# Performance work log

Measured on AMD Instinct MI355X. Metric: run time of the kernel, lower is better.

Reference implementation:

```python
import jax, jax.numpy as jnp
import numpy as np

N_NODES = 50000
N_EDGES = 800000
BASIS = 64
HIDDEN_RO = 128
N_GRAPHS = 512
T = 3


def setup_inputs() -> dict:
    key = jax.random.key(0)
    ks = jax.random.split(key, 12)
    Z = jax.random.randint(ks[0], (N_NODES,), 0, 10)
    edge_index = jax.random.randint(ks[1], (2, N_EDGES), 0, N_NODES)
    edge_attr = jax.random.normal(ks[2], (N_EDGES, BASIS), dtype=jnp.float32)
    batch = jnp.sort(jax.random.randint(ks[3], (N_NODES,), 0, N_GRAPHS))
    s = 1.0 / np.sqrt(BASIS)
    embed = jax.random.normal(ks[4], (10, BASIS), dtype=jnp.float32)
    cfW = jax.random.uniform(ks[5], (BASIS, BASIS), jnp.float32, -s, s)
    cfb = jax.random.uniform(ks[6], (BASIS,), jnp.float32, -s, s)
    dfW = jax.random.uniform(ks[7], (BASIS, BASIS), jnp.float32, -s, s)
    dfb = jax.random.uniform(ks[8], (BASIS,), jnp.float32, -s, s)
    fcW = jax.random.uniform(ks[9], (BASIS, BASIS), jnp.float32, -s, s)  # no bias
    W1 = jax.random.uniform(ks[10], (BASIS, HIDDEN_RO), jnp.float32, -s, s)
    b1 = jnp.zeros((HIDDEN_RO,), jnp.float32)
    W2 = jax.random.uniform(ks[11], (HIDDEN_RO, 4), jnp.float32, -1.0 / np.sqrt(HIDDEN_RO), 1.0 / np.sqrt(HIDDEN_RO))
    b2 = jnp.zeros((4,), jnp.float32)
    return {"Z": Z, "edge_index": edge_index, "edge_attr": edge_attr, "batch": batch,
            "embed": embed, "cfW": cfW, "cfb": cfb, "dfW": dfW, "dfb": dfb, "fcW": fcW,
            "W1": W1, "b1": b1, "W2": W2, "b2": b2}


def reference(Z, edge_index, edge_attr, batch, embed, cfW, cfb, dfW, dfb, fcW, W1, b1, W2, b2):
    src, dst = edge_index[0], edge_index[1]  # x_j gathered from src, aggregated at dst
    C = embed[Z]  # [N, basis]
    # df(edge_attr) does not depend on C; compute once (same math, shared weights)
    d_feat = edge_attr @ dfW + dfb  # [E, basis]
    for _ in range(T):
        c_feat = C[src] @ cfW + cfb            # gather + linear  [E, basis]
        msg = jnp.tanh((c_feat * d_feat) @ fcW)  # [E, basis]
        agg = jax.ops.segment_sum(msg, dst, num_segments=N_NODES)
        C = C + agg
    h = jnp.tanh(C @ W1 + b1) @ W2 + b2        # readout MLP [N, 4]
    return jax.ops.segment_sum(h, batch, num_segments=N_GRAPHS)  # global_add_pool [G, 4]
```

## Files before the change

kernel.cpp:

```cpp
#include <hip/hip_runtime.h>
#include <math.h>

#define N_NODES   50000
#define N_EDGES   800000
#define BASIS     64
#define HIDDEN_RO 128
#define N_GRAPHS  512
#define T_ITERS   3

typedef short s8 __attribute__((ext_vector_type(8)));
typedef float f4 __attribute__((ext_vector_type(4)));

#define MFMA16(a, b, c) __builtin_amdgcn_mfma_f32_16x16x32_bf16(a, b, c, 0, 0, 0)

__device__ __forceinline__ float fast_tanh(float x) {
    float e = __expf(2.0f * x);
    return 1.0f - 2.0f / (e + 1.0f);
}

__device__ __forceinline__ f4 splat4(float x) { f4 v; v[0]=x; v[1]=x; v[2]=x; v[3]=x; return v; }

__device__ __forceinline__ void split8(const float* x, s8& hi, s8& lo) {
    union { unsigned a[4]; s8 v; } H, L;
    #pragma unroll
    for (int j = 0; j < 4; ++j) {
        float e0 = x[2*j], e1 = x[2*j+1];
        unsigned u0 = __float_as_uint(e0), u1 = __float_as_uint(e1);
        H.a[j] = (u0 >> 16) | (u1 & 0xFFFF0000u);
        float l0 = e0 - __uint_as_float(u0 & 0xFFFF0000u);
        float l1 = e1 - __uint_as_float(u1 & 0xFFFF0000u);
        L.a[j] = (__float_as_uint(l0) >> 16) | (__float_as_uint(l1) & 0xFFFF0000u);
    }
    hi = H.v; lo = L.v;
}

__device__ __forceinline__ void packW_dev(const float* __restrict__ W, s8* __restrict__ img, int t) {
    int lane = t & 63, q = lane >> 4, c = lane & 15;
    int f0 = (t >> 6) * 2;
    #pragma unroll
    for (int f = f0; f < f0 + 2; ++f) {
        int ks = f >> 2, g = f & 3;
        float tv[8];
        #pragma unroll
        for (int j = 0; j < 8; ++j)
            tv[j] = W[(ks*32 + q*8 + j) * 64 + g*16 + c];
        s8 hi, lo;
        split8(tv, hi, lo);
        img[f * 64 + lane]       = hi;
        img[(8 + f) * 64 + lane] = lo;
    }
}
__global__ void k_packW(const float* __restrict__ W0, const float* __restrict__ W1,
                        const float* __restrict__ W2, s8* __restrict__ i0,
                        s8* __restrict__ i1, s8* __restrict__ i2) {
    int b = blockIdx.x, t = threadIdx.x;
    if (b == 0) packW_dev(W0, i0, t);
    else if (b == 1) packW_dev(W1, i1, t);
    else packW_dev(W2, i2, t);
}

__global__ void k_init_hist(const int* __restrict__ Z, const float* __restrict__ embed,
                            float* __restrict__ C, const int* __restrict__ dst,
                            int* __restrict__ deg) {
    int i = blockIdx.x * blockDim.x + threadIdx.x;
    if (i < N_NODES * BASIS) { int n = i >> 6, c = i & 63; C[i] = embed[Z[n] * 64 + c]; }
    if (i < N_EDGES) atomicAdd(&deg[dst[i]], 1);
}

__global__ void k_scan(const int* __restrict__ deg, int* __restrict__ off,
                       int* __restrict__ cursor) {
    __shared__ int wsum[16];
    __shared__ int run_s;
    int t = threadIdx.x, lane = t & 63, w = t >> 6;
    if (t == 0) run_s = 0;
    __syncthreads();
    for (int base = 0; base < N_NODES; base += 1024) {
        int i = base + t;
        int v = (i < N_NODES) ? deg[i] : 0;
        int s = v;
        #pragma unroll
        for (int ofs = 1; ofs < 64; ofs <<= 1) {
            int tmp = __shfl_up(s, ofs, 64);
            if (lane >= ofs) s += tmp;
        }
        if (lane == 63) wsum[w] = s;
        __syncthreads();
        if (w == 0) {
            int x = (lane < 16) ? wsum[lane] : 0;
            #pragma unroll
            for (int ofs = 1; ofs < 16; ofs <<= 1) {
                int tmp = __shfl_up(x, ofs, 64);
                if (lane >= ofs) x += tmp;
            }
            if (lane < 16) wsum[lane] = x;
        }
        __syncthreads();
        int run = run_s;
        int wex = (w == 0) ? 0 : wsum[w - 1];
        int incl = run + wex + s;
        if (i < N_NODES) { off[i] = incl - v; cursor[i] = incl - v; }
        __syncthreads();
        if (t == 1023) run_s = incl;
        __syncthreads();
    }
    if (t == 0) off[N_NODES] = run_s;
}

__global__ void k_fill(const int* __restrict__ src, const int* __restrict__ dst,
                       int* __restrict__ cursor, int* __restrict__ slot_e,
                       int* __restrict__ slot_s) {
    int e = blockIdx.x * blockDim.x + threadIdx.x;
    if (e < N_EDGES) {
        int d = dst[e], s = src[e];
        int p = atomicAdd(&cursor[d], 1);
        slot_e[p] = e;
        slot_s[p] = s;
    }
}

template <int MODE>
__global__ __launch_bounds__(256, 4) void k_gemm64L(const float* __restrict__ in,
        const s8* __restrict__ wimg, const float* __restrict__ b,
        const int* __restrict__ slot_e, float* __restrict__ out, int rows) {
    __shared__ s8 LW[1024];
    int t = threadIdx.x;
    for (int i = t; i < 1024; i += 256) LW[i] = wimg[i];
    __syncthreads();
    int lane = t & 63, wv = t >> 6, q = lane >> 4, c = lane & 15;
    float bias[4];
    #pragma unroll
    for (int g = 0; g < 4; ++g) bias[g] = b[g*16 + c];
    int chunks = (rows + 15) >> 4;
    int wave = blockIdx.x * 4 + wv, nw = gridDim.x * 4;
    for (int ch = wave; ch < chunks; ch += nw) {
        int base = ch << 4;
        int row = base + c;
        bool valid = row < rows;
        int r = valid ? row : 0;
        if (MODE == 1) r = slot_e[valid ? row : base];
        const float4* ip = (const float4*)(in + (size_t)r * 64);
        s8 ahi[2], alo[2];
        #pragma unroll
        for (int ks = 0; ks < 2; ++ks) {
            float4 a0 = ip[ks*8 + q*2 + 0];
            float4 a1 = ip[ks*8 + q*2 + 1];
            float xs[8] = {a0.x,a0.y,a0.z,a0.w, a1.x,a1.y,a1.z,a1.w};
            if (!valid) {
                #pragma unroll
                for (int j = 0; j < 8; ++j) xs[j] = 0.0f;
            }
            split8(xs, ahi[ks], alo[ks]);
        }
        f4 acc[4];
        #pragma unroll
        for (int g = 0; g < 4; ++g) acc[g] = splat4(bias[g]);
        #pragma unroll
        for (int ks = 0; ks < 2; ++ks)
            #pragma unroll
            for (int g = 0; g < 4; ++g) {
                s8 wh = LW[(ks*4 + g) * 64 + lane];
                s8 wl = LW[(8 + ks*4 + g) * 64 + lane];
                acc[g] = MFMA16(ahi[ks], wh, acc[g]);
                acc[g] = MFMA16(ahi[ks], wl, acc[g]);
                acc[g] = MFMA16(alo[ks], wh, acc[g]);
            }
        #pragma unroll
        for (int g = 0; g < 4; ++g)
            #pragma unroll
            for (int r2 = 0; r2 < 4; ++r2) {
                int ro = base + q*4 + r2;
                if (ro < rows) out[(size_t)ro * 64 + g*16 + c] = acc[g][r2];
            }
    }
}

__global__ __launch_bounds__(256, 4) void k_mp5(const float* __restrict__ CF,
        const float* __restrict__ DF, const s8* __restrict__ wimg,
        const int* __restrict__ slot_s, const int* __restrict__ off,
        float* __restrict__ C) {
    __shared__ s8 LW[1024];
    int t = threadIdx.x;
    for (int i = t; i < 1024; i += 256) LW[i] = wimg[i];
    __syncthreads();
    int lane = t & 63, wv = t >> 6, q = lane >> 4, c = lane & 15;
    int wave = blockIdx.x * 4 + wv, nw = gridDim.x * 4;
    for (int n = wave; n < N_NODES; n += nw) {
        int beg = off[n], end = off[n + 1];
        if (beg >= end) continue;
        float acc0 = 0.f, acc1 = 0.f, acc2 = 0.f, acc3 = 0.f;
        int sl0 = beg + c; if (sl0 >= end) sl0 = end - 1;
        int srcn = slot_s[sl0];
        #pragma unroll 1
        for (int base = beg; base < end; base += 16) {
            int slot = base + c;
            bool valid = slot < end;
            if (!valid) slot = end - 1;
            int scur = srcn;
            if (base + 16 < end) {
                int s2 = base + 16 + c; if (s2 >= end) s2 = end - 1;
                srcn = slot_s[s2];
            }
            const float4* dp = (const float4*)(DF + (size_t)slot * 64);
            float4 d0 = dp[q*2],     d1 = dp[q*2 + 1];
            float4 d2 = dp[8 + q*2], d3 = dp[8 + q*2 + 1];
            const float4* cp = (const float4*)(CF + (size_t)scur * 64);
            float4 c0 = cp[q*2],     c1 = cp[q*2 + 1];
            float4 c2 = cp[8 + q*2], c3 = cp[8 + q*2 + 1];
            s8 ahi[2], alo[2];
            {
                float xs[8] = {c0.x*d0.x, c0.y*d0.y, c0.z*d0.z, c0.w*d0.w,
                               c1.x*d1.x, c1.y*d1.y, c1.z*d1.z, c1.w*d1.w};
                if (!valid) {
                    #pragma unroll
                    for (int j = 0; j < 8; ++j) xs[j] = 0.0f;
                }
                split8(xs, ahi[0], alo[0]);
                float ys[8] = {c2.x*d2.x, c2.y*d2.y, c2.z*d2.z, c2.w*d2.w,
                               c3.x*d3.x, c3.y*d3.y, c3.z*d3.z, c3.w*d3.w};
                if (!valid) {
                    #pragma unroll
                    for (int j = 0; j < 8; ++j) ys[j] = 0.0f;
                }
                split8(ys, ahi[1], alo[1]);
            }
            f4 d[4];
            #pragma unroll
            for (int g = 0; g < 4; ++g) d[g] = splat4(0.0f);
            #pragma unroll
            for (int ks = 0; ks < 2; ++ks)
                #pragma unroll
                for (int g = 0; g < 4; ++g) {
                    s8 wh = LW[(ks*4 + g) * 64 + lane];
                    s8 wl = LW[(8 + ks*4 + g) * 64 + lane];
                    d[g] = MFMA16(ahi[ks], wh, d[g]);
                    d[g] = MFMA16(ahi[ks], wl, d[g]);
                    d[g] = MFMA16(alo[ks], wh, d[g]);
                }
            acc0 += fast_tanh(d[0][0]) + fast_tanh(d[0][1]) + fast_tanh(d[0][2]) + fast_tanh(d[0][3]);
            acc1 += fast_tanh(d[1][0]) + fast_tanh(d[1][1]) + fast_tanh(d[1][2]) + fast_tanh(d[1][3]);
            acc2 += fast_tanh(d[2][0]) + fast_tanh(d[2][1]) + fast_tanh(d[2][2]) + fast_tanh(d[2][3]);
            acc3 += fast_tanh(d[3][0]) + fast_tanh(d[3][1]) + fast_tanh(d[3][2]) + fast_tanh(d[3][3]);
        }
        acc0 += __shfl_xor(acc0, 16, 64); acc0 += __shfl_xor(acc0, 32, 64);
        acc1 += __shfl_xor(acc1, 16, 64); acc1 += __shfl_xor(acc1, 32, 64);
        acc2 += __shfl_xor(acc2, 16, 64); acc2 += __shfl_xor(acc2, 32, 64);
        acc3 += __shfl_xor(acc3, 16, 64); acc3 += __shfl_xor(acc3, 32, 64);
        float v = (q == 0) ? acc0 : (q == 1) ? acc1 : (q == 2) ? acc2 : acc3;
        C[(size_t)n * 64 + lane] += v;
    }
}

__global__ __launch_bounds__(256) void k_gemm64_fb(const float* __restrict__ in,
        const float* __restrict__ W, const float* __restrict__ b,
        float* __restrict__ out, int rows) {
    int r = blockIdx.x * blockDim.x + threadIdx.x;
    if (r >= rows) return;
    float acc[BASIS];
    #pragma unroll
    for (int c = 0; c < BASIS; ++c) acc[c] = b[c];
    const float4* in4 = (const float4*)(in + (size_t)r * BASIS);
    #pragma unroll 1
    for (int k0 = 0; k0 < 16; ++k0) {
        float4 xv = in4[k0];
        #pragma unroll
        for (int c = 0; c < BASIS; ++c)
            acc[c] += xv.x * W[(4*k0+0)*64+c] + xv.y * W[(4*k0+1)*64+c]
                    + xv.z * W[(4*k0+2)*64+c] + xv.w * W[(4*k0+3)*64+c];
    }
    #pragma unroll
    for (int c = 0; c < BASIS; ++c) out[(size_t)r * BASIS + c] = acc[c];
}
__global__ __launch_bounds__(256) void k_edge_fb(const float* __restrict__ CF,
        const float* __restrict__ ea, const float* __restrict__ dfW,
        const float* __restrict__ dfb, const float* __restrict__ fcW,
        const int* __restrict__ src, const int* __restrict__ dst,
        float* __restrict__ C) {
    int e = blockIdx.x * blockDim.x + threadIdx.x;
    if (e >= N_EDGES) return;
    int s = src[e], d = dst[e];
    float dfeat[BASIS];
    #pragma unroll
    for (int c = 0; c < BASIS; ++c) dfeat[c] = dfb[c];
    const float4* ea4 = (const float4*)(ea + (size_t)e * BASIS);
    #pragma unroll
    for (int k0 = 0; k0 < 16; ++k0) {
        float4 xv = ea4[k0];
        #pragma unroll
        for (int c = 0; c < BASIS; ++c)
            dfeat[c] += xv.x * dfW[(4*k0+0)*64+c] + xv.y * dfW[(4*k0+1)*64+c]
                      + xv.z * dfW[(4*k0+2)*64+c] + xv.w * dfW[(4*k0+3)*64+c];
    }
    const float4* cf4 = (const float4*)(CF + (size_t)s * BASIS);
    float acc[BASIS];
    #pragma unroll
    for (int c = 0; c < BASIS; ++c) acc[c] = 0.0f;
    #pragma unroll
    for (int k0 = 0; k0 < 16; ++k0) {
        float4 a = cf4[k0];
        float x0 = a.x * dfeat[4*k0+0], x1 = a.y * dfeat[4*k0+1];
        float x2 = a.z * dfeat[4*k0+2], x3 = a.w * dfeat[4*k0+3];
        #pragma unroll
        for (int c = 0; c < BASIS; ++c)
            acc[c] += x0 * fcW[(4*k0+0)*64+c] + x1 * fcW[(4*k0+1)*64+c]
                    + x2 * fcW[(4*k0+2)*64+c] + x3 * fcW[(4*k0+3)*64+c];
    }
    float* crow = C + (size_t)d * BASIS;
    #pragma unroll
    for (int c = 0; c < BASIS; ++c) atomicAdd(&crow[c], fast_tanh(acc[c]));
}

__global__ __launch_bounds__(256) void k_readout2(const float* __restrict__ C,
        const float* __restrict__ W1, const float* __restrict__ b1,
        const float* __restrict__ W2, const float* __restrict__ b2,
        const int* __restrict__ batch, float* __restrict__ out) {
    __shared__ float w1[BASIS * HIDDEN_RO];
    __shared__ float xbuf[4][64];
    int t = threadIdx.x;
    for (int i = t; i < BASIS * HIDDEN_RO; i += 256) w1[i] = W1[i];
    __syncthreads();
    int lane = t & 63, wv = t >> 6;
    float b1a = b1[lane], b1b = b1[64 + lane];
    float4 w2a = ((const float4*)W2)[lane];
    float4 w2b = ((const float4*)W2)[64 + lane];
    int wave = blockIdx.x * 4 + wv;
    int nw   = gridDim.x * 4;
    for (int n = wave; n < N_NODES; n += nw) {
        float x = C[(size_t)n * 64 + lane];
        xbuf[wv][lane] = x;
        __builtin_amdgcn_wave_barrier();
        const float4* xb = (const float4*)xbuf[wv];
        float sa = b1a, sb = b1b;
        #pragma unroll
        for (int k4 = 0; k4 < 16; ++k4) {
            float4 xv = xb[k4];
            const float* r0 = &w1[(4*k4 + 0) * HIDDEN_RO];
            const float* r1 = &w1[(4*k4 + 1) * HIDDEN_RO];
            const float* r2 = &w1[(4*k4 + 2) * HIDDEN_RO];
            const float* r3 = &w1[(4*k4 + 3) * HIDDEN_RO];
            sa += xv.x * r0[lane]      + xv.y * r1[lane]
                + xv.z * r2[lane]      + xv.w * r3[lane];
            sb += xv.x * r0[64 + lane] + xv.y * r1[64 + lane]
                + xv.z * r2[64 + lane] + xv.w * r3[64 + lane];
        }
        float ha = fast_tanh(sa), hb = fast_tanh(sb);
        float v0 = ha * w2a.x + hb * w2b.x;
        float v1 = ha * w2a.y + hb * w2b.y;
        float v2 = ha * w2a.z + hb * w2b.z;
        float v3 = ha * w2a.w + hb * w2b.w;
        #pragma unroll
        for (int ofs = 32; ofs >= 1; ofs >>= 1) {
            v0 += __shfl_down(v0, ofs, 64);
            v1 += __shfl_down(v1, ofs, 64);
            v2 += __shfl_down(v2, ofs, 64);
            v3 += __shfl_down(v3, ofs, 64);
        }
        if (lane == 0) {
            int g = batch[n];
            atomicAdd(&out[(size_t)g * 4 + 0], v0);
            atomicAdd(&out[(size_t)g * 4 + 1], v1);
            atomicAdd(&out[(size_t)g * 4 + 2], v2);
            atomicAdd(&out[(size_t)g * 4 + 3], v3);
        }
        __builtin_amdgcn_wave_barrier();
    }
}

extern "C" void kernel_launch(void* const* d_in, const int* in_sizes, int n_in,
                              void* d_out, int out_size, void* d_ws, size_t ws_size,
                              hipStream_t stream) {
    const int*   Z     = (const int*)d_in[0];
    const int*   ei    = (const int*)d_in[1];
    const float* ea    = (const float*)d_in[2];
    const int*   batch = (const int*)d_in[3];
    const float* embed = (const float*)d_in[4];
    const float* cfW   = (const float*)d_in[5];
    const float* cfb   = (const float*)d_in[6];
    const float* dfW   = (const float*)d_in[7];
    const float* dfb   = (const float*)d_in[8];
    const float* fcW   = (const float*)d_in[9];
    const float* W1    = (const float*)d_in[10];
    const float* b1    = (const float*)d_in[11];
    const float* W2    = (const float*)d_in[12];
    const float* b2    = (const float*)d_in[13];
    const int* src = ei;
    const int* dst = ei + N_EDGES;
    float* out = (float*)d_out;

    const size_t bC = (size_t)N_NODES * BASIS * sizeof(float);
    const size_t bE = (size_t)N_EDGES * sizeof(int);
    const size_t bO = (size_t)(N_NODES + 1) * sizeof(int);
    const size_t bI = 1024 * sizeof(s8);
    char* p = (char*)d_ws;
    float* C      = (float*)p;  p += bC;
    float* CF     = (float*)p;  p += bC;
    int*   slotE  = (int*)p;    p += bE;
    int*   slotS  = (int*)p;    p += bE;
    int*   deg    = (int*)p;    p += bO;
    int*   off    = (int*)p;    p += bO;
    int*   cursor = (int*)p;    p += bO;
    p = (char*)(((uintptr_t)p + 255) & ~(uintptr_t)255);
    s8* imgDF = (s8*)p;  p += bI;
    s8* imgCF = (s8*)p;  p += bI;
    s8* imgFC = (s8*)p;  p += bI;
    float* DF = (float*)p;
    const size_t need = (size_t)(p - (char*)d_ws) + (size_t)N_EDGES * BASIS * sizeof(float);
    const bool full = ws_size >= need;

    hipMemsetAsync(d_out, 0, (size_t)out_size * sizeof(float), stream);

    if (full) {
        hipMemsetAsync(deg, 0, bO, stream);
        k_init_hist<<<(N_NODES * BASIS + 255) / 256, 256, 0, stream>>>(Z, embed, C, dst, deg);
        k_packW<<<3, 256, 0, stream>>>(dfW, cfW, fcW, imgDF, imgCF, imgFC);
        k_scan<<<1, 1024, 0, stream>>>(deg, off, cursor);
        k_fill<<<(N_EDGES + 255) / 256, 256, 0, stream>>>(src, dst, cursor, slotE, slotS);
        k_gemm64L<1><<<4096, 256, 0, stream>>>(ea, imgDF, dfb, slotE, DF, N_EDGES);
        for (int t = 0; t < T_ITERS; ++t) {
            k_gemm64L<0><<<800, 256, 0, stream>>>(C, imgCF, cfb, nullptr, CF, N_NODES);
            k_mp5<<<2048, 256, 0, stream>>>(CF, DF, imgFC, slotS, off, C);
        }
    } else {
        k_init_hist<<<(N_NODES * BASIS + 255) / 256, 256, 0, stream>>>(Z, embed, C, dst, (int*)CF);
        for (int t = 0; t < T_ITERS; ++t) {
            k_gemm64_fb<<<(N_NODES + 255) / 256, 256, 0, stream>>>(C, cfW, cfb, CF, N_NODES);
            k_edge_fb<<<(N_EDGES + 255) / 256, 256, 0, stream>>>(CF, ea, dfW, dfb, fcW, src, dst, C);
        }
    }

    k_readout2<<<512, 256, 0, stream>>>(C, W1, b1, W2, b2, batch, out);
}
```

Baseline: 922.6 us.

## Parallelize degree scan across blocks and move readout MLP onto MFMA

Replaces the single-block serial prefix scan over 50k node degrees with a three-kernel multi-block scan (block-local scan, scan of block sums, add-back). Adds a new readout kernel that packs W1 into split-bf16 hi/lo images, computes the 64x128 hidden layer with MFMA, and applies tanh and the 128x4 projection in registers before atomically pooling per graph. Both changes target serial or scalar bottlenecks outside the main message-passing loop, at the cost of two extra launches for the scan and small precision differences from the bf16x3 split.

```diff
diff --git a/kernel.cpp b/kernel.cpp
--- a/kernel.cpp
+++ b/kernel.cpp
@@ -7,6 +7,7 @@
 #define HIDDEN_RO 128
 #define N_GRAPHS  512
 #define T_ITERS   3
+#define NB_SCAN   ((N_NODES + 255) / 256)
 
 typedef short s8 __attribute__((ext_vector_type(8)));
 typedef float f4 __attribute__((ext_vector_type(4)));
@@ -50,13 +51,33 @@
         img[(8 + f) * 64 + lane] = lo;
     }
 }
-__global__ void k_packW(const float* __restrict__ W0, const float* __restrict__ W1,
-                        const float* __restrict__ W2, s8* __restrict__ i0,
-                        s8* __restrict__ i1, s8* __restrict__ i2) {
+
+__device__ __forceinline__ void packW1_dev(const float* __restrict__ W, s8* __restrict__ img, int t) {
+    int lane = t & 63, q = lane >> 4, c = lane & 15;
+    int f0 = (t >> 6) * 4;
+    #pragma unroll
+    for (int f = f0; f < f0 + 4; ++f) {
+        int ks = f >> 3, g = f & 7;
+        float tv[8];
+        #pragma unroll
+        for (int j = 0; j < 8; ++j)
+            tv[j] = W[(ks*32 + q*8 + j) * HIDDEN_RO + g*16 + c];
+        s8 hi, lo;
+        split8(tv, hi, lo);
+        img[f * 64 + lane]        = hi;
+        img[(16 + f) * 64 + lane] = lo;
+    }
+}
+
+__global__ void k_packW(const float* __restrict__ W0, const float* __restrict__ W1m,
+                        const float* __restrict__ W2m, const float* __restrict__ W1ro,
+                        s8* __restrict__ i0, s8* __restrict__ i1, s8* __restrict__ i2,
+                        s8* __restrict__ i3) {
     int b = blockIdx.x, t = threadIdx.x;
     if (b == 0) packW_dev(W0, i0, t);
-    else if (b == 1) packW_dev(W1, i1, t);
-    else packW_dev(W2, i2, t);
+    else if (b == 1) packW_dev(W1m, i1, t);
+    else if (b == 2) packW_dev(W2m, i2, t);
+    else packW1_dev(W1ro, i3, t);
 }
 
 __global__ void k_init_hist(const int* __restrict__ Z, const float* __restrict__ embed,
@@ -67,43 +88,62 @@
     if (i < N_EDGES) atomicAdd(&deg[dst[i]], 1);
 }
 
-__global__ void k_scan(const int* __restrict__ deg, int* __restrict__ off,
-                       int* __restrict__ cursor) {
-    __shared__ int wsum[16];
-    __shared__ int run_s;
+__global__ void k_scan1(const int* __restrict__ deg, int* __restrict__ off,
+                        int* __restrict__ bsum) {
+    __shared__ int ws[4];
+    int b = blockIdx.x, t = threadIdx.x, lane = t & 63, w = t >> 6;
+    int i = b * 256 + t;
+    int v = (i < N_NODES) ? deg[i] : 0;
+    int s = v;
+    #pragma unroll
+    for (int ofs = 1; ofs < 64; ofs <<= 1) {
+        int tmp = __shfl_up(s, ofs, 64);
+        if (lane >= ofs) s += tmp;
+    }
+    if (lane == 63) ws[w] = s;
+    __syncthreads();
+    if (t == 0) {
+        int a = 0;
+        #pragma unroll
+        for (int k = 0; k < 4; ++k) { int x = ws[k]; ws[k] = a; a += x; }
+        bsum[b] = a;
+    }
+    __syncthreads();
+    int excl = ws[w] + s - v;
+    if (i < N_NODES) off[i] = excl;
+}
+
+__global__ void k_scan2(int* __restrict__ bsum) {
+    __shared__ int ws[4];
     int t = threadIdx.x, lane = t & 63, w = t >> 6;
-    if (t == 0) run_s = 0;
-    __syncthreads();
-    for (int base = 0; base < N_NODES; base += 1024) {
-        int i = base + t;
-        int v = (i < N_NODES) ? deg[i] : 0;
-        int s = v;
-        #pragma unroll
-        for (int ofs = 1; ofs < 64; ofs <<= 1) {
-            int tmp = __shfl_up(s, ofs, 64);
-            if (lane >= ofs) s += tmp;
-        }
-        if (lane == 63) wsum[w] = s;
-        __syncthreads();
-        if (w == 0) {
-            int x = (lane < 16) ? wsum[lane] : 0;
-            #pragma unroll
-            for (int ofs = 1; ofs < 16; ofs <<= 1) {
-                int tmp = __shfl_up(x, ofs, 64);
-                if (lane >= ofs) x += tmp;
-            }
-            if (lane < 16) wsum[lane] = x;
-        }
-        __syncthreads();
-        int run = run_s;
-        int wex = (w == 0) ? 0 : wsum[w - 1];
-        int incl = run + wex + s;
-        if (i < N_NODES) { off[i] = incl - v; cursor[i] = incl - v; }
-        __syncthreads();
-        if (t == 1023) run_s = incl;
-        __syncthreads();
-    }
-    if (t == 0) off[N_NODES] = run_s;
+    int v = (t < NB_SCAN) ? bsum[t] : 0;
+    int s = v;
+    #pragma unroll
+    for (int ofs = 1; ofs < 64; ofs <<= 1) {
+        int tmp = __shfl_up(s, ofs, 64);
+        if (lane >= ofs) s += tmp;
+    }
+    if (lane == 63) ws[w] = s;
+    __syncthreads();
+    if (t == 0) {
+        int a = 0;
+        #pragma unroll
+        for (int k = 0; k < 4; ++k) { int x = ws[k]; ws[k] = a; a += x; }
+    }
+    __syncthreads();
+    int excl = ws[w] + s - v;
+    if (t < NB_SCAN) bsum[t] = excl;
+}
+
+__global__ void k_scan3(const int* __restrict__ deg, int* __restrict__ off,
+                        const int* __restrict__ bsum, int* __restrict__ cursor) {
+    int b = blockIdx.x, i = b * 256 + threadIdx.x;
+    if (i < N_NODES) {
+        int val = off[i] + bsum[b];
+        off[i] = val;
+        cursor[i] = val;
+        if (i == N_NODES - 1) off[N_NODES] = val + deg[i];
+    }
 }
 
 __global__ void k_fill(const int* __restrict__ src, const int* __restrict__ dst,
@@ -365,6 +405,96 @@
     }
 }
 
+__global__ __launch_bounds__(256, 2) void k_readout3(const float* __restrict__ C,
+        const s8* __restrict__ wimg, const float* __restrict__ b1,
+        const float* __restrict__ W2, const float* __restrict__ b2,
+        const int* __restrict__ batch, float* __restrict__ out) {
+    __shared__ s8 LW[2048];
+    int t = threadIdx.x;
+    for (int i = t; i < 2048; i += 256) LW[i] = wimg[i];
+    __syncthreads();
+    int lane = t & 63, wv = t >> 6, q = lane >> 4, c = lane & 15;
+    float bias[8];
+    #pragma unroll
+    for (int g = 0; g < 8; ++g) bias[g] = b1[g*16 + c];
+    f4 w2r[8];
+    #pragma unroll
+    for (int g = 0; g < 8; ++g) {
+        float4 w4 = ((const float4*)W2)[g*16 + c];
+        w2r[g][0] = w4.x; w2r[g][1] = w4.y; w2r[g][2] = w4.z; w2r[g][3] = w4.w;
+    }
+    float4 b2v = *(const float4*)b2;
+    int chunks = (N_NODES + 15) >> 4;
+    int wave = blockIdx.x * 4 + wv, nw = gridDim.x * 4;
+    for (int ch = wave; ch < chunks; ch += nw) {
+        int base = ch << 4;
+        int row = base + c;
+        bool valid = row < N_NODES;
+        int r = valid ? row : 0;
+        const float4* ip = (const float4*)(C + (size_t)r * 64);
+        s8 ahi[2], alo[2];
+        #pragma unroll
+        for (int ks = 0; ks < 2; ++ks) {
+            float4 a0 = ip[ks*8 + q*2 + 0];
+            float4 a1 = ip[ks*8 + q*2 + 1];
+            float xs[8] = {a0.x,a0.y,a0.z,a0.w, a1.x,a1.y,a1.z,a1.w};
+            if (!valid) {
+                #pragma unroll
+                for (int j = 0; j < 8; ++j) xs[j] = 0.0f;
+            }
+            split8(xs, ahi[ks], alo[ks]);
+        }
+        f4 acc[8];
+        #pragma unroll
+        for (int g = 0; g < 8; ++g) acc[g] = splat4(bias[g]);
+        #pragma unroll
+        for (int ks = 0; ks < 2; ++ks)
+            #pragma unroll
+            for (int g = 0; g < 8; ++g) {
+                s8 wh = LW[(ks*8 + g) * 64 + lane];
+                s8 wl = LW[(16 + ks*8 + g) * 64 + lane];
+                acc[g] = MFMA16(ahi[ks], wh, acc[g]);
+                acc[g] = MFMA16(ahi[ks], wl, acc[g]);
+                acc[g] = MFMA16(alo[ks], wh, acc[g]);
+            }
+        f4 v4[4];
+        #pragma unroll
+        for (int r2 = 0; r2 < 4; ++r2) v4[r2] = splat4(0.0f);
+        #pragma unroll
+        for (int g = 0; g < 8; ++g)
+            #pragma unroll
+            for (int r2 = 0; r2 < 4; ++r2) {
+                float h = fast_tanh(acc[g][r2]);
+                #pragma unroll
+                for (int j = 0; j < 4; ++j) v4[r2][j] += h * w2r[g][j];
+            }
+        #pragma unroll
+        for (int r2 = 0; r2 < 4; ++r2)
+            #pragma unroll
+            for (int j = 0; j < 4; ++j) {
+                float x = v4[r2][j];
+                x += __shfl_xor(x, 1, 64);
+                x += __shfl_xor(x, 2, 64);
+                x += __shfl_xor(x, 4, 64);
+                x += __shfl_xor(x, 8, 64);
+                v4[r2][j] = x;
+            }
+        if (c == 0) {
+            #pragma unroll
+            for (int r2 = 0; r2 < 4; ++r2) {
+                int ro = base + q*4 + r2;
+                if (ro < N_NODES) {
+                    int g_id = batch[ro];
+                    atomicAdd(&out[(size_t)g_id * 4 + 0], v4[r2][0] + b2v.x);
+                    atomicAdd(&out[(size_t)g_id * 4 + 1], v4[r2][1] + b2v.y);
+                    atomicAdd(&out[(size_t)g_id * 4 + 2], v4[r2][2] + b2v.z);
+                    atomicAdd(&out[(size_t)g_id * 4 + 3], v4[r2][3] + b2v.w);
+                }
+            }
+        }
+    }
+}
+
 extern "C" void kernel_launch(void* const* d_in, const int* in_sizes, int n_in,
                               void* d_out, int out_size, void* d_ws, size_t ws_size,
                               hipStream_t stream) {
@@ -402,6 +532,8 @@
     s8* imgDF = (s8*)p;  p += bI;
     s8* imgCF = (s8*)p;  p += bI;
     s8* imgFC = (s8*)p;  p += bI;
+    s8* imgW1 = (s8*)p;  p += 2048 * sizeof(s8);
+    int* bsum = (int*)p; p += 256 * sizeof(int);
     float* DF = (float*)p;
     const size_t need = (size_t)(p - (char*)d_ws) + (size_t)N_EDGES * BASIS * sizeof(float);
     const bool full = ws_size >= need;
@@ -411,21 +543,23 @@
     if (full) {
         hipMemsetAsync(deg, 0, bO, stream);
         k_init_hist<<<(N_NODES * BASIS + 255) / 256, 256, 0, stream>>>(Z, embed, C, dst, deg);
-        k_packW<<<3, 256, 0, stream>>>(dfW, cfW, fcW, imgDF, imgCF, imgFC);
-        k_scan<<<1, 1024, 0, stream>>>(deg, off, cursor);
+        k_packW<<<4, 256, 0, stream>>>(dfW, cfW, fcW, W1, imgDF, imgCF, imgFC, imgW1);
+        k_scan1<<<NB_SCAN, 256, 0, stream>>>(deg, off, bsum);
+        k_scan2<<<1, 256, 0, stream>>>(bsum);
+        k_scan3<<<NB_SCAN, 256, 0, stream>>>(deg, off, bsum, cursor);
         k_fill<<<(N_EDGES + 255) / 256, 256, 0, stream>>>(src, dst, cursor, slotE, slotS);
         k_gemm64L<1><<<4096, 256, 0, stream>>>(ea, imgDF, dfb, slotE, DF, N_EDGES);
         for (int t = 0; t < T_ITERS; ++t) {
             k_gemm64L<0><<<800, 256, 0, stream>>>(C, imgCF, cfb, nullptr, CF, N_NODES);
             k_mp5<<<2048, 256, 0, stream>>>(CF, DF, imgFC, slotS, off, C);
         }
+        k_readout3<<<1024, 256, 0, stream>>>(C, imgW1, b1, W2, b2, batch, out);
     } else {
         k_init_hist<<<(N_NODES * BASIS + 255) / 256, 256, 0, stream>>>(Z, embed, C, dst, (int*)CF);
         for (int t = 0; t < T_ITERS; ++t) {
             k_gemm64_fb<<<(N_NODES + 255) / 256, 256, 0, stream>>>(C, cfW, cfb, CF, N_NODES);
             k_edge_fb<<<(N_EDGES + 255) / 256, 256, 0, stream>>>(CF, ea, dfW, dfb, fcW, src, dst, C);
         }
-    }
-
-    k_readout2<<<512, 256, 0, stream>>>(C, W1, b1, W2, b2, batch, out);
-}
+        k_readout2<<<512, 256, 0, stream>>>(C, W1, b1, W2, b2, batch, out);
+    }
+}
```

Result: faster. 866.0 us (-6.1%).
